# Performance work log

Hardware: AMD Instinct MI355X
Metric: run time of the kernel (lower is better)

## Reference

```python
import jax, jax.numpy as jnp
import numpy as np

N = 4096
FIN = 256
FOUT = 256
H = 1  # num_heads MUST be 1: edge projections reshape [N,N,H] -> (1,N,N)
NEG_MASK = -1000000.0
LRELU_SLOPE = 0.2
ESP = 1e-06
LN_EPS = 1e-05


def setup_inputs() -> dict:
    key = jax.random.key(0)
    ks = jax.random.split(key, 9)
    nodes_features = jax.random.normal(ks[0], (N, FIN), dtype=jnp.float32)
    degree_matrix = jax.random.normal(ks[1], (N, N), dtype=jnp.float32)
    edges_features_distance = jax.random.uniform(ks[2], (N, N), dtype=jnp.float32)
    edges_features_bond = jax.random.uniform(ks[3], (N, N), dtype=jnp.float32)
    # learned parameters (xavier-ish scale)
    proj_param = jax.random.normal(ks[4], (H, FIN, FOUT), dtype=jnp.float32) * (1.0 / np.sqrt(FIN))
    a_src = jax.random.normal(ks[5], (H, FOUT, 1), dtype=jnp.float32) * (1.0 / np.sqrt(FOUT))
    a_tgt = jax.random.normal(ks[6], (H, FOUT, 1), dtype=jnp.float32) * (1.0 / np.sqrt(FOUT))
    w_dist = jax.random.normal(ks[7], (H, 1), dtype=jnp.float32)  # nn.Linear(1, H).weight
    w_bond = jax.random.normal(ks[8], (H, 1), dtype=jnp.float32)
    return {
        "nodes_features": nodes_features,
        "degree_matrix": degree_matrix,
        "edges_features_distance": edges_features_distance,
        "edges_features_bond": edges_features_bond,
        "proj_param": proj_param,
        "a_src": a_src,
        "a_tgt": a_tgt,
        "w_dist": w_dist,
        "w_bond": w_bond,
        "cutoff": 0,
    }


def reference(nodes_features, degree_matrix, edges_features_distance,
              edges_features_bond, proj_param, a_src, a_tgt, w_dist, w_bond,
              cutoff=0):
    n = nodes_features.shape[0]
    h, fin, fout = proj_param.shape
    # connectivity mask: keep degree where positive, else large negative
    connectivity_mask = jnp.where(degree_matrix > 0, degree_matrix, NEG_MASK)
    # node projection: [H, N, Fout] (dropout is identity in eval)
    proj = jnp.einsum('nf,hfo->hno', nodes_features, proj_param)
    # attention scores: outer-sum of per-node source/target scores
    s_src = jnp.einsum('hno,hoi->hni', proj, a_src)      # [H, N, 1]
    s_tgt = jnp.einsum('hno,hoi->hni', proj, a_tgt)      # [H, N, 1]
    all_scores = jax.nn.leaky_relu(s_src + jnp.swapaxes(s_tgt, 1, 2), LRELU_SLOPE)  # [H,N,N]
    # edge contributions: Linear(1, H) on scalar edge features, reshaped (1,N,N) (H==1)
    dist_c = ((-edges_features_distance)[..., None] * w_dist[:, 0]).reshape(1, n, n)
    bond_c = (edges_features_bond[..., None] * w_bond[:, 0]).reshape(1, n, n)
    all_scores = all_scores + dist_c + bond_c
    # masked softmax over neighbors
    attn = jax.nn.softmax(all_scores + connectivity_mask[None], axis=-1)  # [H,N,N]
    # weighted aggregation
    out = jnp.einsum('hnm,hmo->hno', attn, proj)  # [H, N, Fout]
    # faithful to torch: transpose(2,1) -> [H,Fout,N] then contiguous view(-1,H,Fout)
    out = jnp.transpose(out, (0, 2, 1)).reshape(-1, h, fout)
    # concat heads (skip connection and bias are disabled per init args)
    out = out.reshape(-1, h * fout)
    out = jax.nn.elu(out)  # ELU activation, alpha=1
    # ---- no_grad connectivity update ----
    o = jax.lax.stop_gradient(out)
    dm = jax.lax.stop_gradient(degree_matrix)
    sim = o @ o.T                                        # [N, N]
    decay = -jax.lax.stop_gradient(edges_features_distance)
    upd = jax.nn.sigmoid(sim) * decay * (dm > 0).astype(o.dtype)
    upd = upd + ESP
    mean = jnp.mean(upd, axis=-1, keepdims=True)
    var = jnp.mean(jnp.square(upd - mean), axis=-1, keepdims=True)
    upd = (upd - mean) / jnp.sqrt(var + LN_EPS)          # layer_norm, no affine
    upd = upd + upd.T
    return out, upd
```

## Files before the change

kernel.cpp:

```cpp
#include <hip/hip_runtime.h>


using f32x4  = __attribute__((ext_vector_type(4))) float;
using bf16x8 = __attribute__((ext_vector_type(8))) __bf16;
using bf16x4 = __attribute__((ext_vector_type(4))) __bf16;
using u32x4  = __attribute__((ext_vector_type(4))) unsigned int;

__global__ __launch_bounds__(256) void cvt_nodes_kernel(const float* __restrict__ x,
                                                        __bf16* __restrict__ y) {
  int i = (blockIdx.x * 256 + threadIdx.x) * 4;
  f32x4 v = *(const f32x4*)(x + i);
  bf16x4 o = { (__bf16)v[0], (__bf16)v[1], (__bf16)v[2], (__bf16)v[3] };
  *(bf16x4*)(y + i) = o;
}

__global__ __launch_bounds__(256) void cvt_wt_kernel(const float* __restrict__ w,
                                                     __bf16* __restrict__ wt) {
  int i = blockIdx.x * 256 + threadIdx.x;
  int o = i >> 8, f = i & 255;
  wt[i] = (__bf16)w[f * 256 + o];
}

template<int BM, int BN, int MODE>
__global__ __launch_bounds__(256) void gemm_bf16_kernel(
    const __bf16* __restrict__ A, const __bf16* __restrict__ Bt,
    int M, int N, int K,
    float* __restrict__ outf, __bf16* __restrict__ outb,
    const float* __restrict__ e0, const float* __restrict__ e1,
    const __bf16* __restrict__ axp, float* __restrict__ outt)
{
  constexpr int LDT = 72;
  constexpr int MI = BM / 32;
  constexpr int NI = BN / 32;
  __shared__ alignas(16) __bf16 As[BM * LDT];
  __shared__ alignas(16) __bf16 Bs[BN * LDT];
  const int tid  = threadIdx.x;
  const int lane = tid & 63;
  const int wid  = tid >> 6;
  const int wm0  = (wid >> 1) * (BM / 2);
  const int wn0  = (wid & 1) * (BN / 2);
  const int m0   = blockIdx.x * BM;
  const int n0   = blockIdx.y * BN;
  const int lr   = lane & 15;
  const int lk   = lane >> 4;

  f32x4 acc[MI][NI];
#pragma unroll
  for (int a = 0; a < MI; ++a)
#pragma unroll
    for (int b = 0; b < NI; ++b) acc[a][b] = (f32x4){0.f, 0.f, 0.f, 0.f};

  for (int kt = 0; kt < K; kt += 64) {
    __syncthreads();
    for (int idx = tid; idx < BM * 8; idx += 256) {
      int r = idx >> 3, c = idx & 7;
      u32x4 v = *(const u32x4*)(A + (size_t)(m0 + r) * K + kt + c * 8);
      *(u32x4*)(As + r * LDT + c * 8) = v;
    }
    for (int idx = tid; idx < BN * 8; idx += 256) {
      int r = idx >> 3, c = idx & 7;
      u32x4 v = *(const u32x4*)(Bt + (size_t)(n0 + r) * K + kt + c * 8);
      *(u32x4*)(Bs + r * LDT + c * 8) = v;
    }
    __syncthreads();
#pragma unroll
    for (int kk = 0; kk < 2; ++kk) {
      bf16x8 av[MI], bv[NI];
#pragma unroll
      for (int mi = 0; mi < MI; ++mi)
        av[mi] = *(const bf16x8*)(As + (wm0 + mi * 16 + lr) * LDT + kk * 32 + lk * 8);
#pragma unroll
      for (int ni = 0; ni < NI; ++ni)
        bv[ni] = *(const bf16x8*)(Bs + (wn0 + ni * 16 + lr) * LDT + kk * 32 + lk * 8);
#pragma unroll
      for (int mi = 0; mi < MI; ++mi)
#pragma unroll
        for (int ni = 0; ni < NI; ++ni)
          acc[mi][ni] = __builtin_amdgcn_mfma_f32_16x16x32_bf16(av[mi], bv[ni], acc[mi][ni], 0, 0, 0);
    }
  }

#pragma unroll
  for (int mi = 0; mi < MI; ++mi) {
#pragma unroll
    for (int ni = 0; ni < NI; ++ni) {
#pragma unroll
      for (int j = 0; j < 4; ++j) {
        const int m = m0 + wm0 + mi * 16 + lk * 4 + j;
        const int n = n0 + wn0 + ni * 16 + lr;
        const float v = acc[mi][ni][j];
        if constexpr (MODE == 0) {
          outf[(size_t)m * 256 + n] = v;
          outb[(size_t)n * 4096 + m] = (__bf16)v;
        } else if constexpr (MODE == 2) {
          const size_t idx = (size_t)m * 4096 + n;
          const float d = e0[idx];
          const float g = e1[idx];
          const float s = 1.0f / (1.0f + expf(-v));
          outt[idx] = s * (-d) * (g > 0.f ? 1.0f : 0.0f) + 1e-6f;
        } else {
          const size_t idx = (size_t)m * 4096 + n;
          const float a = (float)axp[idx];
          const float s = 1.0f / (1.0f + expf(-v));
          outt[idx] = s * a + 1e-6f;
        }
      }
    }
  }
}

__global__ __launch_bounds__(512, 4) void fused_attn_kernel(
    const float* __restrict__ dist, const float* __restrict__ bond,
    const float* __restrict__ deg,  const float* __restrict__ ssrc,
    const float* __restrict__ stgt, const float* __restrict__ wdp,
    const float* __restrict__ wbp,  const __bf16* __restrict__ Bt,
    __bf16* __restrict__ partial,   float* __restrict__ Lbuf,
    __bf16* __restrict__ aux)
{
  constexpr int LDT = 72;
  __shared__ alignas(16) __bf16 As[64 * LDT];
  __shared__ alignas(16) __bf16 Bs[256 * LDT];
  const int tid  = threadIdx.x;
  const int lane = tid & 63;
  const int wid  = tid >> 6;
  const int wm0  = (wid >> 2) * 32;
  const int wn0  = (wid & 3) * 64;
  const int m0   = blockIdx.x * 64;
  const int s    = blockIdx.y;
  const int k0   = s * 256;
  const int lr   = lane & 15;
  const int lk   = lane >> 4;

  const int r  = tid >> 3;
  const int c0 = (tid & 7) * 8;
  const float wd = wdp[0], wb = wbp[0];
  const float si = ssrc[m0 + r];

  f32x4 acc[2][4];
#pragma unroll
  for (int a = 0; a < 2; ++a)
#pragma unroll
    for (int b = 0; b < 4; ++b) acc[a][b] = (f32x4){0.f, 0.f, 0.f, 0.f};
  float lsum = 0.f;

  for (int kt = 0; kt < 256; kt += 64) {
    const size_t ebase = (size_t)(m0 + r) * 4096 + k0 + kt + c0;
    f32x4 d0 = *(const f32x4*)(dist + ebase);
    f32x4 d1 = *(const f32x4*)(dist + ebase + 4);
    f32x4 g0 = *(const f32x4*)(deg + ebase);
    f32x4 g1 = *(const f32x4*)(deg + ebase + 4);
    f32x4 b0 = *(const f32x4*)(bond + ebase);
    f32x4 b1 = *(const f32x4*)(bond + ebase + 4);
    f32x4 s0 = *(const f32x4*)(stgt + k0 + kt + c0);
    f32x4 s1 = *(const f32x4*)(stgt + k0 + kt + c0 + 4);
    u32x4 br[4];
#pragma unroll
    for (int i = 0; i < 4; ++i) {
      int idx = i * 512 + tid;
      int n = idx >> 3, seg = idx & 7;
      br[i] = *(const u32x4*)(Bt + (size_t)n * 4096 + k0 + kt + seg * 8);
    }
    __syncthreads();
    bf16x8 pa, ax;
#pragma unroll
    for (int q = 0; q < 8; ++q) {
      const float dd = q < 4 ? d0[q & 3] : d1[q & 3];
      const float gg = q < 4 ? g0[q & 3] : g1[q & 3];
      const float bb = q < 4 ? b0[q & 3] : b1[q & 3];
      const float ss = q < 4 ? s0[q & 3] : s1[q & 3];
      float x = si + ss;
      x = x > 0.f ? x : 0.2f * x;
      x += -dd * wd + bb * wb + (gg > 0.f ? gg : -1000000.0f);
      const float e = expf(x);
      lsum += e;
      pa[q] = (__bf16)e;
      ax[q] = (__bf16)(gg > 0.f ? -dd : 0.0f);
    }
    *(bf16x8*)(As + r * LDT + c0) = pa;
    if (aux) *(bf16x8*)(aux + ebase) = ax;
#pragma unroll
    for (int i = 0; i < 4; ++i) {
      int idx = i * 512 + tid;
      int n = idx >> 3, seg = idx & 7;
      *(u32x4*)(Bs + n * LDT + seg * 8) = br[i];
    }
    __syncthreads();
#pragma unroll
    for (int kk = 0; kk < 2; ++kk) {
      bf16x8 av[2], bv[4];
#pragma unroll
      for (int mi = 0; mi < 2; ++mi)
        av[mi] = *(const bf16x8*)(As + (wm0 + mi * 16 + lr) * LDT + kk * 32 + lk * 8);
#pragma unroll
      for (int ni = 0; ni < 4; ++ni)
        bv[ni] = *(const bf16x8*)(Bs + (wn0 + ni * 16 + lr) * LDT + kk * 32 + lk * 8);
#pragma unroll
      for (int mi = 0; mi < 2; ++mi)
#pragma unroll
        for (int ni = 0; ni < 4; ++ni)
          acc[mi][ni] = __builtin_amdgcn_mfma_f32_16x16x32_bf16(av[mi], bv[ni], acc[mi][ni], 0, 0, 0);
    }
  }

  __bf16* P = partial + (size_t)s * (4096 * 256);
#pragma unroll
  for (int mi = 0; mi < 2; ++mi)
#pragma unroll
    for (int ni = 0; ni < 4; ++ni)
#pragma unroll
      for (int j = 0; j < 4; ++j) {
        const int m = m0 + wm0 + mi * 16 + lk * 4 + j;
        const int n = wn0 + ni * 16 + lr;
        P[(size_t)m * 256 + n] = (__bf16)acc[mi][ni][j];
      }
  lsum += __shfl_xor(lsum, 1, 64);
  lsum += __shfl_xor(lsum, 2, 64);
  lsum += __shfl_xor(lsum, 4, 64);
  if ((tid & 7) == 0) Lbuf[s * 4096 + m0 + r] = lsum;
}

__global__ __launch_bounds__(256) void reduce_elu_kernel(
    const __bf16* __restrict__ partial, const float* __restrict__ Lbuf,
    float* __restrict__ out0, __bf16* __restrict__ E)
{
  __shared__ float tile[64][65];
  __shared__ float invL[64];
  const int tid = threadIdx.x;
  const int m0 = blockIdx.x * 64;
  const int f0 = blockIdx.y * 64;
  if (tid < 64) {
    float ls = 0.f;
#pragma unroll
    for (int s = 0; s < 16; ++s) ls += Lbuf[s * 4096 + m0 + tid];
    invL[tid] = 1.0f / ls;
  }
  f32x4 accv[4];
#pragma unroll
  for (int i = 0; i < 4; ++i) {
    int lin = i * 1024 + tid * 4;
    int r = lin >> 6, c = lin & 63;
    f32x4 sum = (f32x4){0.f, 0.f, 0.f, 0.f};
#pragma unroll
    for (int s = 0; s < 16; ++s) {
      bf16x4 pv = *(const bf16x4*)(partial + (size_t)s * (4096 * 256) +
                                   (size_t)(m0 + r) * 256 + f0 + c);
#pragma unroll
      for (int q = 0; q < 4; ++q) sum[q] += (float)pv[q];
    }
    accv[i] = sum;
  }
  __syncthreads();
#pragma unroll
  for (int i = 0; i < 4; ++i) {
    int lin = i * 1024 + tid * 4;
    int r = lin >> 6, c = lin & 63;
    const float inv = invL[r];
    tile[r][c]     = accv[i][0] * inv;
    tile[r][c + 1] = accv[i][1] * inv;
    tile[r][c + 2] = accv[i][2] * inv;
    tile[r][c + 3] = accv[i][3] * inv;
  }
  __syncthreads();
#pragma unroll
  for (int i = 0; i < 4; ++i) {
    int lin = i * 1024 + tid * 4;
    int rr = lin >> 6, cc = lin & 63;
    f32x4 e;
#pragma unroll
    for (int q = 0; q < 4; ++q) {
      float v = tile[cc + q][rr];
      e[q] = v > 0.f ? v : expm1f(v);
    }
    size_t idx = (size_t)(f0 + rr) * 4096 + m0 + cc;
    *(f32x4*)(out0 + idx) = e;
    bf16x4 eb = { (__bf16)e[0], (__bf16)e[1], (__bf16)e[2], (__bf16)e[3] };
    *(bf16x4*)(E + idx) = eb;
  }
}

__global__ __launch_bounds__(256) void sproj_kernel(const float* __restrict__ proj,
                                                    const float* __restrict__ asrc,
                                                    const float* __restrict__ atgt,
                                                    float* __restrict__ ssrc,
                                                    float* __restrict__ stgt) {
  const int row  = blockIdx.x * 4 + (threadIdx.x >> 6);
  const int lane = threadIdx.x & 63;
  f32x4 p = *(const f32x4*)(proj + (size_t)row * 256 + lane * 4);
  f32x4 a = *(const f32x4*)(asrc + lane * 4);
  f32x4 b = *(const f32x4*)(atgt + lane * 4);
  float d1 = p[0]*a[0] + p[1]*a[1] + p[2]*a[2] + p[3]*a[3];
  float d2 = p[0]*b[0] + p[1]*b[1] + p[2]*b[2] + p[3]*b[3];
#pragma unroll
  for (int o = 32; o; o >>= 1) { d1 += __shfl_xor(d1, o, 64); d2 += __shfl_xor(d2, o, 64); }
  if (lane == 0) { ssrc[row] = d1; stgt[row] = d2; }
}

__global__ __launch_bounds__(256, 4) void stats_kernel(const float* __restrict__ t,
                                                       float* __restrict__ mean,
                                                       float* __restrict__ rstd) {
  const int row = blockIdx.x;
  const int tid = threadIdx.x;
  const float* tr = t + (size_t)row * 4096;
  f32x4 v[4];
#pragma unroll
  for (int u = 0; u < 4; ++u) v[u] = *(const f32x4*)(tr + u * 1024 + tid * 4);
  float s = 0.f, s2 = 0.f;
#pragma unroll
  for (int u = 0; u < 4; ++u)
#pragma unroll
    for (int q = 0; q < 4; ++q) { s += v[u][q]; s2 += v[u][q] * v[u][q]; }
#pragma unroll
  for (int o = 32; o; o >>= 1) { s += __shfl_xor(s, o, 64); s2 += __shfl_xor(s2, o, 64); }
  __shared__ float bs[4], bs2[4];
  if ((tid & 63) == 0) { bs[tid >> 6] = s; bs2[tid >> 6] = s2; }
  __syncthreads();
  if (tid == 0) {
    float S  = bs[0] + bs[1] + bs[2] + bs[3];
    float S2 = bs2[0] + bs2[1] + bs2[2] + bs2[3];
    float m  = S * (1.0f / 4096.0f);
    float var = S2 * (1.0f / 4096.0f) - m * m;
    mean[row] = m;
    rstd[row] = rsqrtf(var + 1e-5f);
  }
}

__global__ __launch_bounds__(256) void finalize_kernel(float* __restrict__ t,
                                                       const float* __restrict__ mean,
                                                       const float* __restrict__ rstd) {
  const int bj = blockIdx.x, bi = blockIdx.y;
  if (bi > bj) return;
  __shared__ float ta[64][65];
  __shared__ float tb[64][65];
  const int tid = threadIdx.x;
#pragma unroll
  for (int i = 0; i < 4; ++i) {
    int lin = i * 1024 + tid * 4;
    int r = lin >> 6, c = lin & 63;
    f32x4 va = *(const f32x4*)(t + (size_t)(bi * 64 + r) * 4096 + bj * 64 + c);
    ta[r][c] = va[0]; ta[r][c+1] = va[1]; ta[r][c+2] = va[2]; ta[r][c+3] = va[3];
  }
  if (bi != bj) {
#pragma unroll
    for (int i = 0; i < 4; ++i) {
      int lin = i * 1024 + tid * 4;
      int r = lin >> 6, c = lin & 63;
      f32x4 vb = *(const f32x4*)(t + (size_t)(bj * 64 + r) * 4096 + bi * 64 + c);
      tb[r][c] = vb[0]; tb[r][c+1] = vb[1]; tb[r][c+2] = vb[2]; tb[r][c+3] = vb[3];
    }
  }
  __syncthreads();
#pragma unroll
  for (int i = 0; i < 4; ++i) {
    int lin = i * 1024 + tid * 4;
    int r = lin >> 6, c = lin & 63;
    int gi = bi * 64 + r, gj = bj * 64 + c;
    const float mi_ = mean[gi], ri_ = rstd[gi];
    f32x4 mj = *(const f32x4*)(mean + gj);
    f32x4 rj = *(const f32x4*)(rstd + gj);
    f32x4 o;
#pragma unroll
    for (int q = 0; q < 4; ++q) {
      float v = (ta[r][c + q] - mi_) * ri_;
      float w = (bi == bj) ? (ta[c + q][r] - mj[q]) * rj[q]
                           : (tb[c + q][r] - mj[q]) * rj[q];
      o[q] = v + w;
    }
    *(f32x4*)(t + (size_t)gi * 4096 + gj) = o;
  }
  if (bi != bj) {
#pragma unroll
    for (int i = 0; i < 4; ++i) {
      int lin = i * 1024 + tid * 4;
      int r = lin >> 6, c = lin & 63;
      int gi = bj * 64 + r, gj = bi * 64 + c;
      const float mi_ = mean[gi], ri_ = rstd[gi];
      f32x4 mj = *(const f32x4*)(mean + gj);
      f32x4 rj = *(const f32x4*)(rstd + gj);
      f32x4 o;
#pragma unroll
      for (int q = 0; q < 4; ++q) {
        float v = (tb[r][c + q] - mi_) * ri_;
        float w = (ta[c + q][r] - mj[q]) * rj[q];
        o[q] = v + w;
      }
      *(f32x4*)(t + (size_t)gi * 4096 + gj) = o;
    }
  }
}

extern "C" void kernel_launch(void* const* d_in, const int* in_sizes, int n_in,
                              void* d_out, int out_size, void* d_ws, size_t ws_size,
                              hipStream_t stream) {
  const float* nodes  = (const float*)d_in[0];
  const float* degree = (const float*)d_in[1];
  const float* dist   = (const float*)d_in[2];
  const float* bond   = (const float*)d_in[3];
  const float* W      = (const float*)d_in[4];
  const float* a_src  = (const float*)d_in[5];
  const float* a_tgt  = (const float*)d_in[6];
  const float* w_dist = (const float*)d_in[7];
  const float* w_bond = (const float*)d_in[8];

  char* ws = (char*)d_ws;
  __bf16* nodesB = (__bf16*)ws;
  __bf16* Wt     = (__bf16*)(ws + (2u << 20));
  __bf16* projT  = (__bf16*)(ws + (2u << 20) + (256u << 10));
  float*  proj   = (float*)(ws + (5u << 20));
  __bf16* E      = (__bf16*)(ws + (9u << 20));
  float*  ssrc   = (float*)(ws + (11u << 20));
  float*  stgt   = ssrc + 4096;
  float*  mean   = stgt + 4096;
  float*  rstd   = mean + 4096;
  float*  Lbuf   = rstd + 4096;

  const bool useAux = ws_size >= (size_t)(44u << 20);
  __bf16* aux = useAux ? (__bf16*)(ws + (12u << 20)) : nullptr;

  float*  out0 = (float*)d_out;
  float*  t    = out0 + (size_t)4096 * 256;
  __bf16* partials = (__bf16*)t;

  cvt_nodes_kernel<<<1024, 256, 0, stream>>>(nodes, nodesB);
  cvt_wt_kernel<<<256, 256, 0, stream>>>(W, Wt);

  gemm_bf16_kernel<64, 64, 0><<<dim3(64, 4), 256, 0, stream>>>(
      nodesB, Wt, 4096, 256, 256, proj, projT, nullptr, nullptr, nullptr, nullptr);

  sproj_kernel<<<1024, 256, 0, stream>>>(proj, a_src, a_tgt, ssrc, stgt);

  fused_attn_kernel<<<dim3(64, 16), 512, 0, stream>>>(
      dist, bond, degree, ssrc, stgt, w_dist, w_bond, projT,
      partials, Lbuf, aux);

  reduce_elu_kernel<<<dim3(64, 4), 256, 0, stream>>>(partials, Lbuf, out0, E);

  if (useAux)
    gemm_bf16_kernel<128, 128, 3><<<dim3(32, 32), 256, 0, stream>>>(
        E, E, 4096, 4096, 256, nullptr, nullptr, nullptr, nullptr, aux, t);
  else
    gemm_bf16_kernel<128, 128, 2><<<dim3(32, 32), 256, 0, stream>>>(
        E, E, 4096, 4096, 256, nullptr, nullptr, dist, degree, nullptr, t);

  stats_kernel<<<4096, 256, 0, stream>>>(t, mean, rstd);

  finalize_kernel<<<dim3(64, 64), 256, 0, stream>>>(t, mean, rstd);
}
```

Baseline: 172.6 us.

## Load B operands directly from global into registers and double-buffer A tile

The fused attention kernel no longer stages the B (projection transpose) tile through shared memory. Each wave now loads its MFMA B fragments straight from global memory into registers, and the A tile of exponentiated scores is double-buffered so only one barrier per k-step is needed. This cuts LDS traffic and footprint (better occupancy) and removes a sync. In exchange, global loads become less coalesced, since each wave reads 16-byte pieces from many rows. The B data is also re-read redundantly by the two wave rows.

```diff
diff --git a/kernel.cpp b/kernel.cpp
--- a/kernel.cpp
+++ b/kernel.cpp
@@ -118,8 +118,7 @@
     __bf16* __restrict__ aux)
 {
   constexpr int LDT = 72;
-  __shared__ alignas(16) __bf16 As[64 * LDT];
-  __shared__ alignas(16) __bf16 Bs[256 * LDT];
+  __shared__ alignas(16) __bf16 As[2][64 * LDT];
   const int tid  = threadIdx.x;
   const int lane = tid & 63;
   const int wid  = tid >> 6;
@@ -143,7 +142,9 @@
     for (int b = 0; b < 4; ++b) acc[a][b] = (f32x4){0.f, 0.f, 0.f, 0.f};
   float lsum = 0.f;
 
-  for (int kt = 0; kt < 256; kt += 64) {
+#pragma unroll
+  for (int it = 0; it < 4; ++it) {
+    const int kt = it * 64;
     const size_t ebase = (size_t)(m0 + r) * 4096 + k0 + kt + c0;
     f32x4 d0 = *(const f32x4*)(dist + ebase);
     f32x4 d1 = *(const f32x4*)(dist + ebase + 4);
@@ -153,14 +154,13 @@
     f32x4 b1 = *(const f32x4*)(bond + ebase + 4);
     f32x4 s0 = *(const f32x4*)(stgt + k0 + kt + c0);
     f32x4 s1 = *(const f32x4*)(stgt + k0 + kt + c0 + 4);
-    u32x4 br[4];
-#pragma unroll
-    for (int i = 0; i < 4; ++i) {
-      int idx = i * 512 + tid;
-      int n = idx >> 3, seg = idx & 7;
-      br[i] = *(const u32x4*)(Bt + (size_t)n * 4096 + k0 + kt + seg * 8);
-    }
-    __syncthreads();
+    bf16x8 bv[2][4];
+#pragma unroll
+    for (int kk = 0; kk < 2; ++kk)
+#pragma unroll
+      for (int ni = 0; ni < 4; ++ni)
+        bv[kk][ni] = *(const bf16x8*)(Bt + (size_t)(wn0 + ni * 16 + lr) * 4096 +
+                                      k0 + kt + kk * 32 + lk * 8);
     bf16x8 pa, ax;
 #pragma unroll
     for (int q = 0; q < 8; ++q) {
@@ -176,30 +176,23 @@
       pa[q] = (__bf16)e;
       ax[q] = (__bf16)(gg > 0.f ? -dd : 0.0f);
     }
-    *(bf16x8*)(As + r * LDT + c0) = pa;
+    __bf16* Ab = As[it & 1];
+    *(bf16x8*)(Ab + r * LDT + c0) = pa;
     if (aux) *(bf16x8*)(aux + ebase) = ax;
-#pragma unroll
-    for (int i = 0; i < 4; ++i) {
-      int idx = i * 512 + tid;
-      int n = idx >> 3, seg = idx & 7;
-      *(u32x4*)(Bs + n * LDT + seg * 8) = br[i];
-    }
     __syncthreads();
-#pragma unroll
-    for (int kk = 0; kk < 2; ++kk) {
-      bf16x8 av[2], bv[4];
+    bf16x8 av[2][2];
+#pragma unroll
+    for (int kk = 0; kk < 2; ++kk)
 #pragma unroll
       for (int mi = 0; mi < 2; ++mi)
-        av[mi] = *(const bf16x8*)(As + (wm0 + mi * 16 + lr) * LDT + kk * 32 + lk * 8);
-#pragma unroll
-      for (int ni = 0; ni < 4; ++ni)
-        bv[ni] = *(const bf16x8*)(Bs + (wn0 + ni * 16 + lr) * LDT + kk * 32 + lk * 8);
+        av[kk][mi] = *(const bf16x8*)(Ab + (wm0 + mi * 16 + lr) * LDT + kk * 32 + lk * 8);
+#pragma unroll
+    for (int kk = 0; kk < 2; ++kk)
 #pragma unroll
       for (int mi = 0; mi < 2; ++mi)
 #pragma unroll
         for (int ni = 0; ni < 4; ++ni)
-          acc[mi][ni] = __builtin_amdgcn_mfma_f32_16x16x32_bf16(av[mi], bv[ni], acc[mi][ni], 0, 0, 0);
-    }
+          acc[mi][ni] = __builtin_amdgcn_mfma_f32_16x16x32_bf16(av[kk][mi], bv[kk][ni], acc[mi][ni], 0, 0, 0);
   }
 
   __bf16* P = partial + (size_t)s * (4096 * 256);
```

Measured after the change: 198.4 us. +15.0%, slower.
